# Optimization experiments

Hardware: AMD Instinct MI355X
Metric: run time of the kernel (lower is better)

Reference implementation:

```python
import jax, jax.numpy as jnp
import numpy as np

B, S, H = 4, 2048, 768
NUM_POS = B * (S // 4)  # fixed count of positive clc_label entries (2048, even)
NEG_BIG = -1000000000.0


def setup_inputs() -> dict:
    key = jax.random.key(0)
    k1, k2, k3, k4, k5 = jax.random.split(key, 5)
    encoded_states = jax.random.normal(k1, (B, S, H), dtype=jnp.float32)
    # sorted cell-ids -> contiguous segments for the equality mask
    indicator = jnp.sort(jax.random.randint(k2, (B, S), 0, 256, dtype=jnp.int32), axis=-1)
    # clc_label: first S//4 positions per row are positive targets (class ids in [1,S)),
    # last S//2 positions are -1 (attendable keys), rest 0 (ignored)
    pos_labels = jax.random.randint(k3, (B, S // 4), 1, S, dtype=jnp.int32)
    clc_label = jnp.zeros((B, S), dtype=jnp.int32)
    clc_label = clc_label.at[:, : S // 4].set(pos_labels)
    clc_label = clc_label.at[:, S // 2:].set(-1)
    # uniform_linear params (torch Linear: y = x @ W.T + b)
    W = jax.random.normal(k4, (H, H), dtype=jnp.float32) / np.sqrt(H)
    b = jax.random.normal(k5, (H,), dtype=jnp.float32) * 0.01
    return {"encoded_states": encoded_states, "W": W, "b": b,
            "indicator": indicator, "clc_label": clc_label}


def _ce(logits, labels):
    # mean cross entropy; all labels are > 0 here so ignore_index=0 never triggers
    logp = jax.nn.log_softmax(logits, axis=-1)
    return -jnp.take_along_axis(logp, labels[:, None], axis=1).mean()


def reference(encoded_states, W, b, indicator, clc_label):
    # indicator-equality mask matmul == within-segment sum (the segment-reduce emulation)
    seg_mask = (indicator[:, :, None] == indicator[:, None, :]).astype(encoded_states.dtype)  # [B,S,S]
    agg = jnp.einsum("bij,bjh->bih", seg_mask, encoded_states)  # [B,S,H]
    # Q and K use the SAME linear on the same input -> compute once
    proj = jnp.tanh(agg @ W.T + b)  # [B,S,H]
    scores = jnp.einsum("bih,bjh->bij", proj, proj)  # [B,S,S]
    # attend only to positions where clc_label < 0
    allow = (clc_label < 0)[:, None, :]  # [B,1,S]
    scores = scores + jnp.where(allow, 0.0, NEG_BIG).astype(scores.dtype)
    flat = scores.reshape(-1, S)          # [B*S, S]
    labels = clc_label.reshape(-1)        # [B*S]
    pos_idx = jnp.nonzero(labels > 0, size=NUM_POS)[0]  # row-major order == torch bool-indexing
    logits = flat[pos_idx]                # [NUM_POS, S]
    labs = labels[pos_idx]                # [NUM_POS]
    sep_logits, sep_labels = logits[0::2], labs[0::2]
    tok_logits, tok_labels = logits[1::2], labs[1::2]
    sep_loss = _ce(sep_logits, sep_labels)
    tok_loss = _ce(tok_logits, tok_labels)
    sep_correct = jnp.sum((jnp.argmax(sep_logits, axis=-1).astype(jnp.int32) == sep_labels).astype(jnp.float32))
    tok_correct = jnp.sum((jnp.argmax(tok_logits, axis=-1).astype(jnp.int32) == tok_labels).astype(jnp.float32))
    sep_count = jnp.asarray(sep_logits.shape[0] + 1e-6, dtype=jnp.float32)
    tok_count = jnp.asarray(tok_logits.shape[0] + 1e-6, dtype=jnp.float32)
    return ((sep_loss, sep_correct, sep_count), (tok_loss, tok_correct, tok_count))
```

## Files before the change

### kernel.cpp

```cpp
#include <hip/hip_runtime.h>
#include <math.h>
#include <limits.h>

#define BB 4
#define SS 2048
#define HH 768
#define MAXSEG 256
#define NUM_POS (BB*(SS/4))
#define NEG_BIG -1000000000.0f

typedef _Float16 f16x8 __attribute__((ext_vector_type(8)));
typedef _Float16 f16x4 __attribute__((ext_vector_type(4)));
typedef float    f32x4 __attribute__((ext_vector_type(4)));

__global__ __launch_bounds__(256) void k_scanW(
    const int* __restrict__ ind, const int* __restrict__ clc,
    const float* __restrict__ W, _Float16* __restrict__ Wh,
    int* __restrict__ seg_id, int* __restrict__ seg_start,
    int* __restrict__ nseg, int* __restrict__ pos_local, int* __restrict__ pos_cnt,
    int* __restrict__ allowCnt, int* __restrict__ firstAllow)
{
  int t = threadIdx.x;
  if (blockIdx.x >= BB) {
    int idx = (blockIdx.x - BB)*256 + t;
    float4 v = ((const float4*)W)[idx];
    f16x4 h;
    h[0] = (_Float16)v.x; h[1] = (_Float16)v.y;
    h[2] = (_Float16)v.z; h[3] = (_Float16)v.w;
    *(f16x4*)(Wh + (size_t)idx*4) = h;
    return;
  }
  int b = blockIdx.x;
  int lane = t & 63, wid = t >> 6;
  __shared__ int sInd[SS];
  __shared__ int sWave[4];
  __shared__ int sAC[MAXSEG];
  __shared__ int sFA[MAXSEG];
  for (int i = t; i < SS; i += 256) sInd[i] = ind[b*SS + i];
  sAC[t] = 0; sFA[t] = INT_MAX;
  __syncthreads();

  int i0 = t * 8;
  int f[8], cv[8];
  int lsum = 0;
  #pragma unroll
  for (int u = 0; u < 8; u++) {
    int i = i0 + u;
    f[u] = (i == 0) ? 0 : (sInd[i] != sInd[i-1]);
    cv[u] = clc[b*SS + i];
    lsum += f[u];
  }
  int x = lsum;
  #pragma unroll
  for (int off = 1; off < 64; off <<= 1) {
    int v = __shfl_up(x, off, 64);
    if (lane >= off) x += v;
  }
  if (lane == 63) sWave[wid] = x;
  __syncthreads();
  int base = 0;
  for (int w = 0; w < wid; w++) base += sWave[w];
  int run = base + x - lsum;
  int rid[8];
  #pragma unroll
  for (int u = 0; u < 8; u++) {
    int i = i0 + u;
    run += f[u];
    rid[u] = run;
    seg_id[b*SS + i] = run;
    if (f[u] || i == 0) seg_start[b*(MAXSEG+1) + run] = i;
  }
  if (t == 255) { nseg[b] = run + 1; seg_start[b*(MAXSEG+1) + run + 1] = SS; }

  #pragma unroll
  for (int u = 0; u < 8; u++) {
    if (cv[u] < 0) {
      atomicAdd(&sAC[rid[u]], 1);
      atomicMin(&sFA[rid[u]], i0 + u);
    }
  }
  __syncthreads();
  allowCnt[b*MAXSEG + t]   = sAC[t];
  firstAllow[b*MAXSEG + t] = sFA[t];

  int psum = 0;
  int p[8];
  #pragma unroll
  for (int u = 0; u < 8; u++) { p[u] = (cv[u] > 0) ? 1 : 0; psum += p[u]; }
  x = psum;
  #pragma unroll
  for (int off = 1; off < 64; off <<= 1) {
    int v = __shfl_up(x, off, 64);
    if (lane >= off) x += v;
  }
  __syncthreads();
  if (lane == 63) sWave[wid] = x;
  __syncthreads();
  base = 0;
  for (int w = 0; w < wid; w++) base += sWave[w];
  int rank = base + x - psum;
  #pragma unroll
  for (int u = 0; u < 8; u++) {
    if (p[u]) { pos_local[b*SS + rank] = i0 + u; rank++; }
  }
  if (t == 255) pos_cnt[b] = rank;
}

__global__ __launch_bounds__(256) void k_segsum(
    const float* __restrict__ es,
    const int* __restrict__ seg_start, const int* __restrict__ nseg,
    _Float16* __restrict__ segsum_h)
{
  int blk = blockIdx.x, t = threadIdx.x;
  int b = blk >> 8, s = blk & 255;
  _Float16* o = segsum_h + ((size_t)b*MAXSEG + s)*HH;
  if (s >= nseg[b]) {
    o[t] = (_Float16)0.f; o[t+256] = (_Float16)0.f; o[t+512] = (_Float16)0.f;
    return;
  }
  int st = seg_start[b*(MAXSEG+1) + s];
  int en = seg_start[b*(MAXSEG+1) + s + 1];
  const float* base = es + (size_t)b*SS*HH;
  float a0 = 0.f, a1 = 0.f, a2 = 0.f;
  float b0 = 0.f, b1 = 0.f, b2 = 0.f;
  float c0 = 0.f, c1 = 0.f, c2 = 0.f;
  float d0 = 0.f, d1 = 0.f, d2 = 0.f;
  int i = st;
  for (; i + 4 <= en; i += 4) {
    const float* r0 = base + (size_t)i*HH;
    const float* r1 = r0 + HH;
    const float* r2 = r1 + HH;
    const float* r3 = r2 + HH;
    a0 += r0[t]; a1 += r0[t+256]; a2 += r0[t+512];
    b0 += r1[t]; b1 += r1[t+256]; b2 += r1[t+512];
    c0 += r2[t]; c1 += r2[t+256]; c2 += r2[t+512];
    d0 += r3[t]; d1 += r3[t+256]; d2 += r3[t+512];
  }
  for (; i < en; i++) {
    const float* r = base + (size_t)i*HH;
    a0 += r[t]; a1 += r[t+256]; a2 += r[t+512];
  }
  o[t]     = (_Float16)((a0 + b0) + (c0 + d0));
  o[t+256] = (_Float16)((a1 + b1) + (c1 + d1));
  o[t+512] = (_Float16)((a2 + b2) + (c2 + d2));
}

__global__ __launch_bounds__(256) void k_gemmU(
    const _Float16* __restrict__ Ah, const _Float16* __restrict__ Wh,
    const float* __restrict__ bias, _Float16* __restrict__ Uh)
{
  int tid = threadIdx.x;
  int w = tid >> 6, lane = tid & 63;
  int tile = blockIdx.x*4 + w;
  int tm = tile / 24, tn = tile % 24;
  int rb = tm*32, cb = tn*32;
  int m0 = lane & 15, quad = lane >> 4;
  const _Float16* A0 = Ah + (size_t)(rb + m0)*HH + quad*8;
  const _Float16* A1 = A0 + (size_t)16*HH;
  const _Float16* B0 = Wh + (size_t)(cb + m0)*HH + quad*8;
  const _Float16* B1 = B0 + (size_t)16*HH;
  f32x4 acc00 = {0.f,0.f,0.f,0.f}, acc01 = {0.f,0.f,0.f,0.f};
  f32x4 acc10 = {0.f,0.f,0.f,0.f}, acc11 = {0.f,0.f,0.f,0.f};
  #pragma unroll 4
  for (int k0 = 0; k0 < HH; k0 += 32) {
    f16x8 a0 = *(const f16x8*)(A0 + k0);
    f16x8 a1 = *(const f16x8*)(A1 + k0);
    f16x8 b0 = *(const f16x8*)(B0 + k0);
    f16x8 b1 = *(const f16x8*)(B1 + k0);
    acc00 = __builtin_amdgcn_mfma_f32_16x16x32_f16(a0, b0, acc00, 0, 0, 0);
    acc01 = __builtin_amdgcn_mfma_f32_16x16x32_f16(a0, b1, acc01, 0, 0, 0);
    acc10 = __builtin_amdgcn_mfma_f32_16x16x32_f16(a1, b0, acc10, 0, 0, 0);
    acc11 = __builtin_amdgcn_mfma_f32_16x16x32_f16(a1, b1, acc11, 0, 0, 0);
  }
  float bc0 = bias[cb + m0], bc1 = bias[cb + 16 + m0];
  int r0 = rb + quad*4;
  #pragma unroll
  for (int i = 0; i < 4; i++) {
    Uh[(size_t)(r0+i)*HH    + cb + m0]      = (_Float16)tanhf(acc00[i] + bc0);
    Uh[(size_t)(r0+i)*HH    + cb + 16 + m0] = (_Float16)tanhf(acc01[i] + bc1);
    Uh[(size_t)(r0+16+i)*HH + cb + m0]      = (_Float16)tanhf(acc10[i] + bc0);
    Uh[(size_t)(r0+16+i)*HH + cb + 16 + m0] = (_Float16)tanhf(acc11[i] + bc1);
  }
}

__global__ __launch_bounds__(256) void k_gram(
    const _Float16* __restrict__ Uh, float* __restrict__ G)
{
  int tid = threadIdx.x;
  int w = tid >> 6, lane = tid & 63;
  int tile = blockIdx.x*4 + w;
  int b = tile >> 8, rem = tile & 255;
  int rb = (rem >> 4)*16, cb = (rem & 15)*16;
  int m0 = lane & 15, quad = lane >> 4;
  const _Float16* Ub = Uh + (size_t)b*MAXSEG*HH;
  const _Float16* A0 = Ub + (size_t)(rb + m0)*HH + quad*8;
  const _Float16* B0 = Ub + (size_t)(cb + m0)*HH + quad*8;
  f32x4 acc = {0.f,0.f,0.f,0.f};
  #pragma unroll 4
  for (int k0 = 0; k0 < HH; k0 += 32) {
    f16x8 a  = *(const f16x8*)(A0 + k0);
    f16x8 bb = *(const f16x8*)(B0 + k0);
    acc = __builtin_amdgcn_mfma_f32_16x16x32_f16(a, bb, acc, 0, 0, 0);
  }
  float* Gb = G + (size_t)b*MAXSEG*MAXSEG;
  int r0 = rb + quad*4;
  #pragma unroll
  for (int i = 0; i < 4; i++)
    Gb[(size_t)(r0+i)*MAXSEG + cb + m0] = acc[i];
}

__global__ __launch_bounds__(256) void k_seglse(
    const float* __restrict__ G, const int* __restrict__ allowCnt,
    const int* __restrict__ firstAllow, const int* __restrict__ nseg,
    float* __restrict__ lse, int* __restrict__ amax)
{
  int lane = threadIdx.x & 63, wid = threadIdx.x >> 6;
  int row = blockIdx.x * 4 + wid;
  int b = row >> 8, si = row & 255;
  if (si >= nseg[b]) return;
  const float* g = G + ((size_t)b*MAXSEG + si)*MAXSEG;
  const int* ac = allowCnt + b*MAXSEG;
  const int* fa = firstAllow + b*MAXSEG;

  float gv[4]; int av[4], fv[4];
  #pragma unroll
  for (int q = 0; q < 4; q++) {
    int s = lane + 64*q;
    gv[q] = g[s]; av[q] = ac[s]; fv[q] = fa[s];
  }
  float m = -INFINITY;
  #pragma unroll
  for (int q = 0; q < 4; q++) if (av[q] > 0) m = fmaxf(m, gv[q]);
  #pragma unroll
  for (int off = 32; off > 0; off >>= 1) m = fmaxf(m, __shfl_xor(m, off, 64));
  float s = 0.f;
  #pragma unroll
  for (int q = 0; q < 4; q++) if (av[q] > 0) s += (float)av[q] * expf(gv[q] - m);
  #pragma unroll
  for (int off = 32; off > 0; off >>= 1) s += __shfl_xor(s, off, 64);
  float bv = -INFINITY; int bi = INT_MAX;
  #pragma unroll
  for (int q = 0; q < 4; q++) {
    if (av[q] > 0 && (gv[q] > bv || (gv[q] == bv && fv[q] < bi))) { bv = gv[q]; bi = fv[q]; }
  }
  #pragma unroll
  for (int off = 32; off > 0; off >>= 1) {
    float ov = __shfl_xor(bv, off, 64);
    int   oi = __shfl_xor(bi, off, 64);
    if (ov > bv || (ov == bv && oi < bi)) { bv = ov; bi = oi; }
  }
  if (lane == 0) {
    lse[row]  = m + logf(s);
    amax[row] = bi;
  }
}

__global__ __launch_bounds__(256) void k_posfinal(
    const float* __restrict__ G, const int* __restrict__ seg_id,
    const int* __restrict__ clc, const int* __restrict__ pos_local,
    const int* __restrict__ pos_cnt, const float* __restrict__ lse,
    const int* __restrict__ amax, float* __restrict__ out)
{
  __shared__ int sBase[BB+1];
  __shared__ float sL0[4], sC0[4], sL1[4], sC1[4];
  int t = threadIdx.x;
  if (t == 0) {
    int acc = 0; sBase[0] = 0;
    for (int b = 0; b < BB; b++) { acc += pos_cnt[b]; sBase[b+1] = acc; }
  }
  __syncthreads();
  int total = sBase[BB];
  if (total > NUM_POS) total = NUM_POS;

  int rs[8]; bool ok[8]; int bv[8];
  #pragma unroll
  for (int u = 0; u < 8; u++) {
    rs[u] = t + 256*u;
    ok[u] = rs[u] < total;
    int b = 0;
    if (ok[u]) { while (b < BB-1 && rs[u] >= sBase[b+1]) b++; }
    bv[u] = b;
  }
  int iv[8];
  #pragma unroll
  for (int u = 0; u < 8; u++)
    iv[u] = ok[u] ? pos_local[bv[u]*SS + (rs[u] - sBase[bv[u]])] : 0;
  int Lv[8], sv[8];
  #pragma unroll
  for (int u = 0; u < 8; u++) {
    Lv[u] = ok[u] ? clc[bv[u]*SS + iv[u]] : 0;
    sv[u] = ok[u] ? seg_id[bv[u]*SS + iv[u]] : 0;
  }
  int sLv[8], cLv[8];
  #pragma unroll
  for (int u = 0; u < 8; u++) {
    sLv[u] = ok[u] ? seg_id[bv[u]*SS + Lv[u]] : 0;
    cLv[u] = ok[u] ? clc[bv[u]*SS + Lv[u]] : 0;
  }
  float gv[8], lv[8]; int av[8];
  #pragma unroll
  for (int u = 0; u < 8; u++) {
    gv[u] = ok[u] ? G[((size_t)bv[u]*MAXSEG + sv[u])*MAXSEG + sLv[u]] : 0.f;
    lv[u] = ok[u] ? lse[bv[u]*MAXSEG + sv[u]] : 0.f;
    av[u] = ok[u] ? amax[bv[u]*MAXSEG + sv[u]] : -1;
  }

  float l0 = 0.f, c0 = 0.f, l1 = 0.f, c1 = 0.f;
  #pragma unroll
  for (int u = 0; u < 8; u++) {
    if (!ok[u]) continue;
    float vL = gv[u] + (cLv[u] < 0 ? 0.0f : NEG_BIG);
    float loss = lv[u] - vL;
    float corr = (av[u] == Lv[u]) ? 1.0f : 0.0f;
    if (rs[u] & 1) { l1 += loss; c1 += corr; } else { l0 += loss; c0 += corr; }
  }

  int lane = t & 63, wid = t >> 6;
  #pragma unroll
  for (int off = 32; off > 0; off >>= 1) {
    l0 += __shfl_down(l0, off, 64);
    c0 += __shfl_down(c0, off, 64);
    l1 += __shfl_down(l1, off, 64);
    c1 += __shfl_down(c1, off, 64);
  }
  if (lane == 0) { sL0[wid] = l0; sC0[wid] = c0; sL1[wid] = l1; sC1[wid] = c1; }
  __syncthreads();
  if (t == 0) {
    float L0 = sL0[0]+sL0[1]+sL0[2]+sL0[3];
    float C0 = sC0[0]+sC0[1]+sC0[2]+sC0[3];
    float L1 = sL1[0]+sL1[1]+sL1[2]+sL1[3];
    float C1 = sC1[0]+sC1[1]+sC1[2]+sC1[3];
    float n = (float)(NUM_POS/2);
    out[0] = L0 / n;
    out[1] = C0;
    out[2] = n + 1e-6f;
    out[3] = L1 / n;
    out[4] = C1;
    out[5] = n + 1e-6f;
  }
}

extern "C" void kernel_launch(void* const* d_in, const int* in_sizes, int n_in,
                              void* d_out, int out_size, void* d_ws, size_t ws_size,
                              hipStream_t stream)
{
  const float* es   = (const float*)d_in[0];
  const float* W    = (const float*)d_in[1];
  const float* bias = (const float*)d_in[2];
  const int*   ind  = (const int*)d_in[3];
  const int*   clc  = (const int*)d_in[4];
  float* out = (float*)d_out;

  char* ws = (char*)d_ws;
  int*   nseg       = (int*)(ws + 0);
  int*   pos_cnt    = (int*)(ws + 256);
  int*   seg_start  = (int*)(ws + 1024);
  int*   seg_id     = (int*)(ws + 8192);
  int*   pos_local  = (int*)(ws + 40960);
  int*   allowCnt   = (int*)(ws + 73728);
  int*   firstAllow = (int*)(ws + 77824);
  float* lse        = (float*)(ws + 81920);
  int*   amax       = (int*)(ws + 86016);
  _Float16* segsum_h = (_Float16*)(ws + 90112);
  _Float16* Wh       = (_Float16*)(ws + 1662976);
  _Float16* Uh       = (_Float16*)(ws + 2842624);
  float*    G        = (float*)(ws + 4415488);

  k_scanW<<<BB + 576, 256, 0, stream>>>(ind, clc, W, Wh, seg_id, seg_start,
                                        nseg, pos_local, pos_cnt, allowCnt, firstAllow);
  k_segsum<<<BB*MAXSEG, 256, 0, stream>>>(es, seg_start, nseg, segsum_h);
  k_gemmU<<<192, 256, 0, stream>>>(segsum_h, Wh, bias, Uh);
  k_gram<<<256, 256, 0, stream>>>(Uh, G);
  k_seglse<<<(BB*MAXSEG)/4, 256, 0, stream>>>(G, allowCnt, firstAllow, nseg, lse, amax);
  k_posfinal<<<1, 256, 0, stream>>>(G, seg_id, clc, pos_local, pos_cnt, lse, amax, out);
}
```

Baseline: 121.1 us.

## Split segment sums across four thread groups, rebalance gemm blocks, vectorize seglse loads

The segment-sum kernel now runs 1024 threads per segment. Each of four 256-thread groups sums a quarter of the segment's rows, and the partial sums are combined through shared memory. The goal is more memory-level parallelism on the bandwidth-bound reduction over encoded_states. The U gemm moves to 256 blocks of 3 waves instead of 192 blocks of 4, spreading tiles over more CUs. The seglse kernel loads its inputs as float4/int4 vectors, which changes which element indices each lane owns but keeps the reductions equivalent.

```diff
diff --git a/kernel.cpp b/kernel.cpp
--- a/kernel.cpp
+++ b/kernel.cpp
@@ -106,52 +106,63 @@
   if (t == 255) pos_cnt[b] = rank;
 }
 
-__global__ __launch_bounds__(256) void k_segsum(
+__global__ __launch_bounds__(1024) void k_segsum(
     const float* __restrict__ es,
     const int* __restrict__ seg_start, const int* __restrict__ nseg,
     _Float16* __restrict__ segsum_h)
 {
+  __shared__ float sP[4][HH];
   int blk = blockIdx.x, t = threadIdx.x;
   int b = blk >> 8, s = blk & 255;
   _Float16* o = segsum_h + ((size_t)b*MAXSEG + s)*HH;
   if (s >= nseg[b]) {
-    o[t] = (_Float16)0.f; o[t+256] = (_Float16)0.f; o[t+512] = (_Float16)0.f;
+    if (t < HH) o[t] = (_Float16)0.f;
     return;
   }
+  int g = t >> 8, tt = t & 255;
   int st = seg_start[b*(MAXSEG+1) + s];
   int en = seg_start[b*(MAXSEG+1) + s + 1];
+  int len = en - st;
+  int q = (len + 3) >> 2;
+  int gs = st + g*q;
+  int ge = gs + q; if (ge > en) ge = en;
   const float* base = es + (size_t)b*SS*HH;
   float a0 = 0.f, a1 = 0.f, a2 = 0.f;
   float b0 = 0.f, b1 = 0.f, b2 = 0.f;
   float c0 = 0.f, c1 = 0.f, c2 = 0.f;
   float d0 = 0.f, d1 = 0.f, d2 = 0.f;
-  int i = st;
-  for (; i + 4 <= en; i += 4) {
+  int i = gs;
+  for (; i + 4 <= ge; i += 4) {
     const float* r0 = base + (size_t)i*HH;
     const float* r1 = r0 + HH;
     const float* r2 = r1 + HH;
     const float* r3 = r2 + HH;
-    a0 += r0[t]; a1 += r0[t+256]; a2 += r0[t+512];
-    b0 += r1[t]; b1 += r1[t+256]; b2 += r1[t+512];
-    c0 += r2[t]; c1 += r2[t+256]; c2 += r2[t+512];
-    d0 += r3[t]; d1 += r3[t+256]; d2 += r3[t+512];
-  }
-  for (; i < en; i++) {
+    a0 += r0[tt]; a1 += r0[tt+256]; a2 += r0[tt+512];
+    b0 += r1[tt]; b1 += r1[tt+256]; b2 += r1[tt+512];
+    c0 += r2[tt]; c1 += r2[tt+256]; c2 += r2[tt+512];
+    d0 += r3[tt]; d1 += r3[tt+256]; d2 += r3[tt+512];
+  }
+  for (; i < ge; i++) {
     const float* r = base + (size_t)i*HH;
-    a0 += r[t]; a1 += r[t+256]; a2 += r[t+512];
-  }
-  o[t]     = (_Float16)((a0 + b0) + (c0 + d0));
-  o[t+256] = (_Float16)((a1 + b1) + (c1 + d1));
-  o[t+512] = (_Float16)((a2 + b2) + (c2 + d2));
-}
-
-__global__ __launch_bounds__(256) void k_gemmU(
+    a0 += r[tt]; a1 += r[tt+256]; a2 += r[tt+512];
+  }
+  sP[g][tt]     = (a0 + b0) + (c0 + d0);
+  sP[g][tt+256] = (a1 + b1) + (c1 + d1);
+  sP[g][tt+512] = (a2 + b2) + (c2 + d2);
+  __syncthreads();
+  if (t < HH) {
+    float v = (sP[0][t] + sP[1][t]) + (sP[2][t] + sP[3][t]);
+    o[t] = (_Float16)v;
+  }
+}
+
+__global__ __launch_bounds__(192) void k_gemmU(
     const _Float16* __restrict__ Ah, const _Float16* __restrict__ Wh,
     const float* __restrict__ bias, _Float16* __restrict__ Uh)
 {
   int tid = threadIdx.x;
   int w = tid >> 6, lane = tid & 63;
-  int tile = blockIdx.x*4 + w;
+  int tile = blockIdx.x*3 + w;
   int tm = tile / 24, tn = tile % 24;
   int rb = tm*32, cb = tn*32;
   int m0 = lane & 15, quad = lane >> 4;
@@ -222,26 +233,27 @@
   const int* ac = allowCnt + b*MAXSEG;
   const int* fa = firstAllow + b*MAXSEG;
 
-  float gv[4]; int av[4], fv[4];
-  #pragma unroll
-  for (int q = 0; q < 4; q++) {
-    int s = lane + 64*q;
-    gv[q] = g[s]; av[q] = ac[s]; fv[q] = fa[s];
-  }
+  float4 gv = ((const float4*)g)[lane];
+  int4   av = ((const int4*)ac)[lane];
+  int4   fv = ((const int4*)fa)[lane];
+  float gvv[4] = {gv.x, gv.y, gv.z, gv.w};
+  int   avv[4] = {av.x, av.y, av.z, av.w};
+  int   fvv[4] = {fv.x, fv.y, fv.z, fv.w};
+
   float m = -INFINITY;
   #pragma unroll
-  for (int q = 0; q < 4; q++) if (av[q] > 0) m = fmaxf(m, gv[q]);
+  for (int q = 0; q < 4; q++) if (avv[q] > 0) m = fmaxf(m, gvv[q]);
   #pragma unroll
   for (int off = 32; off > 0; off >>= 1) m = fmaxf(m, __shfl_xor(m, off, 64));
   float s = 0.f;
   #pragma unroll
-  for (int q = 0; q < 4; q++) if (av[q] > 0) s += (float)av[q] * expf(gv[q] - m);
+  for (int q = 0; q < 4; q++) if (avv[q] > 0) s += (float)avv[q] * expf(gvv[q] - m);
   #pragma unroll
   for (int off = 32; off > 0; off >>= 1) s += __shfl_xor(s, off, 64);
   float bv = -INFINITY; int bi = INT_MAX;
   #pragma unroll
   for (int q = 0; q < 4; q++) {
-    if (av[q] > 0 && (gv[q] > bv || (gv[q] == bv && fv[q] < bi))) { bv = gv[q]; bi = fv[q]; }
+    if (avv[q] > 0 && (gvv[q] > bv || (gvv[q] == bv && fvv[q] < bi))) { bv = gvv[q]; bi = fvv[q]; }
   }
   #pragma unroll
   for (int off = 32; off > 0; off >>= 1) {
@@ -368,8 +380,8 @@
 
   k_scanW<<<BB + 576, 256, 0, stream>>>(ind, clc, W, Wh, seg_id, seg_start,
                                         nseg, pos_local, pos_cnt, allowCnt, firstAllow);
-  k_segsum<<<BB*MAXSEG, 256, 0, stream>>>(es, seg_start, nseg, segsum_h);
-  k_gemmU<<<192, 256, 0, stream>>>(segsum_h, Wh, bias, Uh);
+  k_segsum<<<BB*MAXSEG, 1024, 0, stream>>>(es, seg_start, nseg, segsum_h);
+  k_gemmU<<<256, 192, 0, stream>>>(segsum_h, Wh, bias, Uh);
   k_gram<<<256, 256, 0, stream>>>(Uh, G);
   k_seglse<<<(BB*MAXSEG)/4, 256, 0, stream>>>(G, allowCnt, firstAllow, nseg, lse, amax);
   k_posfinal<<<1, 256, 0, stream>>>(G, seg_id, clc, pos_local, pos_cnt, lse, amax, out);
```

Result: faster. 117.4 us (-3.1%).
